# Optimization experiments

Measured on AMD Instinct MI355X. Metric: run time of the kernel, lower is better.

The kernel has to match this reference:

```python
import jax, jax.numpy as jnp
import numpy as np

N_RES = 4096
N_PAIRS = 500000

def setup_inputs() -> dict:
    key = jax.random.key(0)
    k1, k2, k3 = jax.random.split(key, 3)
    ca_coords = jax.random.normal(k1, (N_RES, 3), dtype=jnp.float32) * 10.0
    K = jax.random.uniform(k2, (N_RES, N_RES), dtype=jnp.float32)
    pairs = jax.random.randint(k3, (N_PAIRS, 2), 0, N_RES, dtype=jnp.int64)
    return {"ca_coords": ca_coords, "K": K, "pairs": pairs}


def _reconstruct_backbone(ca):
    # vectorized version of reconstruct_backbone_atoms
    n = ca.shape[0]
    vec = ca[1:] - ca[:-1]                                  # (n-1,3)
    unit = vec / (jnp.linalg.norm(vec, axis=-1, keepdims=True) + 1e-8)
    # N atoms: n_coords[i] = ca[i] - 0.38*unit(ca[i]-ca[i-1]); n_coords[0] uses unit[0]
    n_coords = jnp.concatenate([ca[:1] - 0.38 * unit[:1], ca[1:] - 0.38 * unit], axis=0)
    # C atoms: c_coords[i] = ca[i] + 0.38*unit(ca[i+1]-ca[i]); c_coords[-1] uses unit[-1]
    c_coords = jnp.concatenate([ca[:-1] + 0.38 * unit, ca[-1:] + 0.38 * unit[-1:]], axis=0)
    # O atoms: perpendicular to (C-CA, N-CA) plane, last residue special-cased
    vec_n = n_coords[:-1] - ca[:-1]
    vec_c = c_coords[:-1] - ca[:-1]
    perp = jnp.cross(vec_c, vec_n)
    pnorm = jnp.linalg.norm(perp, axis=-1, keepdims=True)
    perp = jnp.where(pnorm > 1e-6, perp / jnp.maximum(pnorm, 1e-12), perp)
    o_body = c_coords[:-1] + 1.24 * perp
    o_last = c_coords[-1:] + jnp.array([[0.0, 1.24, 0.0]], dtype=ca.dtype)
    o_coords = jnp.concatenate([o_body, o_last], axis=0)
    return n_coords, c_coords, o_coords


def _pairwise_dist(x, y):
    # safe cdist: sqrt clamped so diagonal zeros stay differentiable
    sq = jnp.sum((x[:, None, :] - y[None, :, :]) ** 2, axis=-1)
    return jnp.sqrt(jnp.maximum(sq, 1e-12))


def reference(ca_coords, K, pairs):
    n = ca_coords.shape[0]

    # --- bond energy (weight=30): mean((|ca[i+1]-ca[i]| - 3.8)^2) ---
    d_bond = jnp.linalg.norm(ca_coords[1:] - ca_coords[:-1], axis=-1)
    e_bond = 30.0 * jnp.mean((d_bond - 3.8) ** 2)

    # --- clash energy (weight=50): mean(relu(3.2 - d_pair)^2) ---
    dv = ca_coords[pairs[:, 0]] - ca_coords[pairs[:, 1]]
    d_pair = jnp.sqrt(jnp.maximum(jnp.sum(dv ** 2, axis=-1), 1e-12))
    e_clash = 50.0 * jnp.mean(jax.nn.relu(3.2 - d_pair) ** 2)

    # --- contact energy (weight=5): mean((D - 8*(1-K))^2) over full NxN ---
    D = _pairwise_dist(ca_coords, ca_coords)
    target = 8.0 * (1.0 - K)
    e_contact = 5.0 * jnp.mean((D - target) ** 2)

    # --- hydrogen bond energy (weight=4) from reconstructed backbone ---
    n_coords, c_coords, o_coords = _reconstruct_backbone(ca_coords)
    ideal = 2.95
    hb = jnp.float32(0.0)
    # double loop i, j in [i+2, i+6) -> offsets 2..5, vectorized per offset
    for off in (2, 3, 4, 5):
        d = jnp.linalg.norm(o_coords[: n - off] - n_coords[off:], axis=-1)
        pen = jnp.exp(-(((d - ideal) / 0.3) ** 2))
        hb = hb - 0.5 * jnp.sum(jnp.where((d > 2.5) & (d < 3.5), pen, 0.0))
    e_hb = 4.0 * hb / (n * n)

    return e_bond + e_clash + e_contact + e_hb
```

## Files before the change

kernel.cpp:

```cpp
#include <hip/hip_runtime.h>
#include <math.h>

#define NRES   4096
#define TROWS  8
#define GRID   (NRES / TROWS)
#define HB_BLOCKS (NRES / 256)
#define PSTRIDE (GRID * 256)

typedef int i32x2 __attribute__((ext_vector_type(2)));

__device__ __forceinline__ float wave_sum(float v) {
#pragma unroll
    for (int off = 32; off > 0; off >>= 1) v += __shfl_down(v, off, 64);
    return v;
}

__device__ __forceinline__ float fsqrt(float x) { return __builtin_amdgcn_sqrtf(x); }

__device__ __forceinline__ float c4(float4 kv, float4 cx, float4 cy, float4 cz,
                                    float xi, float yi, float zi, float s) {
    float dx, dy, dz, D, t;
    dx = xi - cx.x; dy = yi - cy.x; dz = zi - cz.x;
    D  = fsqrt(fmaf(dx, dx, fmaf(dy, dy, dz * dz)));
    t  = fmaf(8.f, kv.x, D - 8.f);
    s  = fmaf(t, t, s);

    dx = xi - cx.y; dy = yi - cy.y; dz = zi - cz.y;
    D  = fsqrt(fmaf(dx, dx, fmaf(dy, dy, dz * dz)));
    t  = fmaf(8.f, kv.y, D - 8.f);
    s  = fmaf(t, t, s);

    dx = xi - cx.z; dy = yi - cy.z; dz = zi - cz.z;
    D  = fsqrt(fmaf(dx, dx, fmaf(dy, dy, dz * dz)));
    t  = fmaf(8.f, kv.z, D - 8.f);
    s  = fmaf(t, t, s);

    dx = xi - cx.w; dy = yi - cy.w; dz = zi - cz.w;
    D  = fsqrt(fmaf(dx, dx, fmaf(dy, dy, dz * dz)));
    t  = fmaf(8.f, kv.w, D - 8.f);
    s  = fmaf(t, t, s);
    return s;
}

__global__ __launch_bounds__(256, 2) void energy_kernel(const float* __restrict__ ca,
                                                        const float* __restrict__ K,
                                                        const int* __restrict__ pairs,
                                                        float4* __restrict__ partial,
                                                        int npairs) {
    __shared__ float sx[NRES], sy[NRES], sz[NRES];
    __shared__ float red[4][4];
    const int tid = threadIdx.x;
    const int b   = blockIdx.x;

    const int rbase = b * TROWS;
    const float* Kt = K + (size_t)rbase * NRES;
    const int j0 = tid << 2;

    float4 va[TROWS], vb[TROWS];
#pragma unroll
    for (int r = 0; r < TROWS; ++r)
        va[r] = *(const float4*)(Kt + (size_t)r * NRES + j0);

    const int pbase = b * 256 + tid;
    const i32x2* pairs2 = (const i32x2*)pairs;
    i32x2 pr0 = pairs2[pbase];
    i32x2 pr1 = pairs2[pbase + PSTRIDE];
    i32x2 pr2 = pairs2[pbase + 2 * PSTRIDE];
    const bool has3 = (pbase + 3 * PSTRIDE) < npairs;
    i32x2 pr3 = has3 ? pairs2[pbase + 3 * PSTRIDE] : (i32x2){0, 0};

    for (int j = tid; j < NRES; j += 256) {
        sx[j] = ca[3 * j + 0];
        sy[j] = ca[3 * j + 1];
        sz[j] = ca[3 * j + 2];
    }
    __syncthreads();

    float xi[TROWS], yi[TROWS], zi[TROWS];
#pragma unroll
    for (int r = 0; r < TROWS; ++r) {
        xi[r] = sx[rbase + r]; yi[r] = sy[rbase + r]; zi[r] = sz[rbase + r];
    }

    float contact = 0.f, contact2 = 0.f;
#pragma unroll
    for (int c = 0; c < 4; ++c) {
        const int jc = j0 + (c << 10);
        float4* cur = (c & 1) ? vb : va;
        float4* nxt = (c & 1) ? va : vb;
        if (c < 3) {
            const int jn = j0 + ((c + 1) << 10);
#pragma unroll
            for (int r = 0; r < TROWS; ++r)
                nxt[r] = *(const float4*)(Kt + (size_t)r * NRES + jn);
        }
        const float4 cx = *(const float4*)&sx[jc];
        const float4 cy = *(const float4*)&sy[jc];
        const float4 cz = *(const float4*)&sz[jc];
#pragma unroll
        for (int r = 0; r < TROWS; r += 2) {
            contact  = c4(cur[r],     cx, cy, cz, xi[r],     yi[r],     zi[r],     contact);
            contact2 = c4(cur[r + 1], cx, cy, cz, xi[r + 1], yi[r + 1], zi[r + 1], contact2);
        }
    }
    contact += contact2;

    float clash = 0.f;
    {
        float dx, dy, dz, d, r;
        dx = sx[pr0.x] - sx[pr0.y]; dy = sy[pr0.x] - sy[pr0.y]; dz = sz[pr0.x] - sz[pr0.y];
        d = fsqrt(fmaxf(fmaf(dx, dx, fmaf(dy, dy, dz * dz)), 1e-12f));
        r = fmaxf(3.2f - d, 0.f); clash = fmaf(r, r, clash);

        dx = sx[pr1.x] - sx[pr1.y]; dy = sy[pr1.x] - sy[pr1.y]; dz = sz[pr1.x] - sz[pr1.y];
        d = fsqrt(fmaxf(fmaf(dx, dx, fmaf(dy, dy, dz * dz)), 1e-12f));
        r = fmaxf(3.2f - d, 0.f); clash = fmaf(r, r, clash);

        dx = sx[pr2.x] - sx[pr2.y]; dy = sy[pr2.x] - sy[pr2.y]; dz = sz[pr2.x] - sz[pr2.y];
        d = fsqrt(fmaxf(fmaf(dx, dx, fmaf(dy, dy, dz * dz)), 1e-12f));
        r = fmaxf(3.2f - d, 0.f); clash = fmaf(r, r, clash);

        if (has3) {
            dx = sx[pr3.x] - sx[pr3.y]; dy = sy[pr3.x] - sy[pr3.y]; dz = sz[pr3.x] - sz[pr3.y];
            d = fsqrt(fmaxf(fmaf(dx, dx, fmaf(dy, dy, dz * dz)), 1e-12f));
            r = fmaxf(3.2f - d, 0.f); clash = fmaf(r, r, clash);
        }
    }

    float bond = 0.f, hb = 0.f;
    if (b < HB_BLOCKS) {
        const int i = b * 256 + tid;
        const int n = NRES;

        if (i < n - 1) {
            float dx = sx[i+1]-sx[i], dy = sy[i+1]-sy[i], dz = sz[i+1]-sz[i];
            float d  = sqrtf(fmaf(dx, dx, fmaf(dy, dy, dz * dz)));
            float t  = d - 3.8f;
            bond = t * t;
        }

        if (i < n - 2) {
            float cax = sx[i], cay = sy[i], caz = sz[i];
            float vx = sx[i+1]-cax, vy = sy[i+1]-cay, vz = sz[i+1]-caz;
            float inv = 1.f / (sqrtf(vx*vx + vy*vy + vz*vz) + 1e-8f);
            float ux = vx*inv, uy = vy*inv, uz = vz*inv;

            float upx, upy, upz;
            if (i == 0) { upx = ux; upy = uy; upz = uz; }
            else {
                float wx = cax-sx[i-1], wy = cay-sy[i-1], wz = caz-sz[i-1];
                float inv2 = 1.f / (sqrtf(wx*wx + wy*wy + wz*wz) + 1e-8f);
                upx = wx*inv2; upy = wy*inv2; upz = wz*inv2;
            }

            float vcx = 0.38f*ux,  vcy = 0.38f*uy,  vcz = 0.38f*uz;
            float vnx = -0.38f*upx, vny = -0.38f*upy, vnz = -0.38f*upz;
            float px = vcy*vnz - vcz*vny;
            float py = vcz*vnx - vcx*vnz;
            float pz = vcx*vny - vcy*vnx;
            float pn = sqrtf(px*px + py*py + pz*pz);
            if (pn > 1e-6f) {
                float ipn = 1.f / fmaxf(pn, 1e-12f);
                px *= ipn; py *= ipn; pz *= ipn;
            }
            float ox = cax + vcx + 1.24f*px;
            float oy = cay + vcy + 1.24f*py;
            float oz = caz + vcz + 1.24f*pz;

#pragma unroll
            for (int off = 2; off <= 5; ++off) {
                int jj = i + off;
                if (jj < n) {
                    float cjx = sx[jj], cjy = sy[jj], cjz = sz[jj];
                    float qx = cjx-sx[jj-1], qy = cjy-sy[jj-1], qz = cjz-sz[jj-1];
                    float invq = 1.f / (sqrtf(qx*qx + qy*qy + qz*qz) + 1e-8f);
                    float njx = cjx - 0.38f*qx*invq;
                    float njy = cjy - 0.38f*qy*invq;
                    float njz = cjz - 0.38f*qz*invq;
                    float ddx = ox-njx, ddy = oy-njy, ddz = oz-njz;
                    float d = sqrtf(ddx*ddx + ddy*ddy + ddz*ddz);
                    if (d > 2.5f && d < 3.5f) {
                        float z = (d - 2.95f) * (1.0f / 0.3f);
                        hb -= 0.5f * expf(-z*z);
                    }
                }
            }
        }
    }

    float vbo = wave_sum(bond);
    float vcl = wave_sum(clash);
    float vco = wave_sum(contact);
    float vhb = wave_sum(hb);
    const int wave = tid >> 6;
    if ((tid & 63) == 0) {
        red[wave][0] = vbo; red[wave][1] = vcl; red[wave][2] = vco; red[wave][3] = vhb;
    }
    __syncthreads();
    if (tid == 0) {
        float4 o;
        o.x = red[0][0] + red[1][0] + red[2][0] + red[3][0];
        o.y = red[0][1] + red[1][1] + red[2][1] + red[3][1];
        o.z = red[0][2] + red[1][2] + red[2][2] + red[3][2];
        o.w = red[0][3] + red[1][3] + red[2][3] + red[3][3];
        partial[b] = o;
    }
}

__global__ __launch_bounds__(256) void finalize_kernel(const float4* __restrict__ partial,
                                                       float* __restrict__ out,
                                                       int n, int npairs) {
    __shared__ float red[4][4];
    const int tid = threadIdx.x;
    float vb = 0.f, vc = 0.f, vk = 0.f, vh = 0.f;
#pragma unroll
    for (int s = 0; s < GRID; s += 256) {
        float4 a = partial[tid + s];
        vb += a.x; vc += a.y; vk += a.z; vh += a.w;
    }
    vb = wave_sum(vb); vc = wave_sum(vc); vk = wave_sum(vk); vh = wave_sum(vh);
    const int wave = tid >> 6;
    if ((tid & 63) == 0) {
        red[wave][0] = vb; red[wave][1] = vc; red[wave][2] = vk; red[wave][3] = vh;
    }
    __syncthreads();
    if (tid == 0) {
        float bond    = red[0][0] + red[1][0] + red[2][0] + red[3][0];
        float clash   = red[0][1] + red[1][1] + red[2][1] + red[3][1];
        float contact = red[0][2] + red[1][2] + red[2][2] + red[3][2];
        float hb      = red[0][3] + red[1][3] + red[2][3] + red[3][3];
        float inv_nn  = 1.f / ((float)n * (float)n);
        out[0] = 30.f * bond / (float)(n - 1)
               + 50.f * clash / (float)npairs
               + 5.f  * contact * inv_nn
               + 4.f  * hb * inv_nn;
    }
}

extern "C" void kernel_launch(void* const* d_in, const int* in_sizes, int n_in,
                              void* d_out, int out_size, void* d_ws, size_t ws_size,
                              hipStream_t stream) {
    const float* ca    = (const float*)d_in[0];
    const float* K     = (const float*)d_in[1];
    const int*   pairs = (const int*)d_in[2];
    float* out = (float*)d_out;
    float4* partial = (float4*)d_ws;

    int n      = in_sizes[0] / 3;
    int npairs = in_sizes[2] / 2;

    energy_kernel<<<GRID, 256, 0, stream>>>(ca, K, pairs, partial, npairs);
    finalize_kernel<<<1, 256, 0, stream>>>(partial, out, n, npairs);
}
```

Measured before the change: 101.8 us.

## Drop shared-memory coordinate staging and halve rows per block

Removes the per-block copy of all 4096 CA coordinates into LDS and its barrier. Column coordinates are now read straight from global memory as float4 loads and de-interleaved in registers, while pair and H-bond lookups become global gathers. Rows per block drop from 8 to 4, which doubles the grid, and launch bounds are raised to allow more blocks per CU. The aim is to cut redundant LDS staging work and raise occupancy, at the cost of more global and cache traffic for the coordinate gathers.

```diff
diff --git a/kernel.cpp b/kernel.cpp
--- a/kernel.cpp
+++ b/kernel.cpp
@@ -2,7 +2,7 @@
 #include <math.h>
 
 #define NRES   4096
-#define TROWS  8
+#define TROWS  4
 #define GRID   (NRES / TROWS)
 #define HB_BLOCKS (NRES / 256)
 #define PSTRIDE (GRID * 256)
@@ -16,6 +16,11 @@
 }
 
 __device__ __forceinline__ float fsqrt(float x) { return __builtin_amdgcn_sqrtf(x); }
+
+__device__ __forceinline__ void ldp(const float* __restrict__ ca, int i,
+                                    float& x, float& y, float& z) {
+    x = ca[3 * i]; y = ca[3 * i + 1]; z = ca[3 * i + 2];
+}
 
 __device__ __forceinline__ float c4(float4 kv, float4 cx, float4 cy, float4 cz,
                                     float xi, float yi, float zi, float s) {
@@ -42,12 +47,11 @@
     return s;
 }
 
-__global__ __launch_bounds__(256, 2) void energy_kernel(const float* __restrict__ ca,
+__global__ __launch_bounds__(256, 4) void energy_kernel(const float* __restrict__ ca,
                                                         const float* __restrict__ K,
                                                         const int* __restrict__ pairs,
                                                         float4* __restrict__ partial,
                                                         int npairs) {
-    __shared__ float sx[NRES], sy[NRES], sz[NRES];
     __shared__ float red[4][4];
     const int tid = threadIdx.x;
     const int b   = blockIdx.x;
@@ -56,72 +60,67 @@
     const float* Kt = K + (size_t)rbase * NRES;
     const int j0 = tid << 2;
 
-    float4 va[TROWS], vb[TROWS];
+    float4 va[TROWS], vbuf[TROWS];
 #pragma unroll
     for (int r = 0; r < TROWS; ++r)
         va[r] = *(const float4*)(Kt + (size_t)r * NRES + j0);
+
+    float4 la[3], lb[3];
+#pragma unroll
+    for (int q = 0; q < 3; ++q)
+        la[q] = *(const float4*)(ca + 3 * j0 + 4 * q);
 
     const int pbase = b * 256 + tid;
     const i32x2* pairs2 = (const i32x2*)pairs;
     i32x2 pr0 = pairs2[pbase];
-    i32x2 pr1 = pairs2[pbase + PSTRIDE];
-    i32x2 pr2 = pairs2[pbase + 2 * PSTRIDE];
-    const bool has3 = (pbase + 3 * PSTRIDE) < npairs;
-    i32x2 pr3 = has3 ? pairs2[pbase + 3 * PSTRIDE] : (i32x2){0, 0};
-
-    for (int j = tid; j < NRES; j += 256) {
-        sx[j] = ca[3 * j + 0];
-        sy[j] = ca[3 * j + 1];
-        sz[j] = ca[3 * j + 2];
-    }
-    __syncthreads();
+    const bool has1 = (pbase + PSTRIDE) < npairs;
+    i32x2 pr1 = has1 ? pairs2[pbase + PSTRIDE] : (i32x2){0, 0};
 
     float xi[TROWS], yi[TROWS], zi[TROWS];
 #pragma unroll
-    for (int r = 0; r < TROWS; ++r) {
-        xi[r] = sx[rbase + r]; yi[r] = sy[rbase + r]; zi[r] = sz[rbase + r];
-    }
+    for (int r = 0; r < TROWS; ++r)
+        ldp(ca, rbase + r, xi[r], yi[r], zi[r]);
 
     float contact = 0.f, contact2 = 0.f;
 #pragma unroll
     for (int c = 0; c < 4; ++c) {
-        const int jc = j0 + (c << 10);
-        float4* cur = (c & 1) ? vb : va;
-        float4* nxt = (c & 1) ? va : vb;
+        float4* cur  = (c & 1) ? vbuf : va;
+        float4* nxt  = (c & 1) ? va : vbuf;
+        float4* curc = (c & 1) ? lb : la;
+        float4* nxtc = (c & 1) ? la : lb;
         if (c < 3) {
             const int jn = j0 + ((c + 1) << 10);
 #pragma unroll
             for (int r = 0; r < TROWS; ++r)
                 nxt[r] = *(const float4*)(Kt + (size_t)r * NRES + jn);
-        }
-        const float4 cx = *(const float4*)&sx[jc];
-        const float4 cy = *(const float4*)&sy[jc];
-        const float4 cz = *(const float4*)&sz[jc];
-#pragma unroll
-        for (int r = 0; r < TROWS; r += 2) {
-            contact  = c4(cur[r],     cx, cy, cz, xi[r],     yi[r],     zi[r],     contact);
-            contact2 = c4(cur[r + 1], cx, cy, cz, xi[r + 1], yi[r + 1], zi[r + 1], contact2);
-        }
+#pragma unroll
+            for (int q = 0; q < 3; ++q)
+                nxtc[q] = *(const float4*)(ca + 3 * jn + 4 * q);
+        }
+        const float4 cx = make_float4(curc[0].x, curc[0].w, curc[1].z, curc[2].y);
+        const float4 cy = make_float4(curc[0].y, curc[1].x, curc[1].w, curc[2].z);
+        const float4 cz = make_float4(curc[0].z, curc[1].y, curc[2].x, curc[2].w);
+
+        contact  = c4(cur[0], cx, cy, cz, xi[0], yi[0], zi[0], contact);
+        contact2 = c4(cur[1], cx, cy, cz, xi[1], yi[1], zi[1], contact2);
+        contact  = c4(cur[2], cx, cy, cz, xi[2], yi[2], zi[2], contact);
+        contact2 = c4(cur[3], cx, cy, cz, xi[3], yi[3], zi[3], contact2);
     }
     contact += contact2;
 
     float clash = 0.f;
     {
-        float dx, dy, dz, d, r;
-        dx = sx[pr0.x] - sx[pr0.y]; dy = sy[pr0.x] - sy[pr0.y]; dz = sz[pr0.x] - sz[pr0.y];
+        float ax, ay, az, bx, by, bz, dx, dy, dz, d, r;
+        ldp(ca, pr0.x, ax, ay, az);
+        ldp(ca, pr0.y, bx, by, bz);
+        dx = ax - bx; dy = ay - by; dz = az - bz;
         d = fsqrt(fmaxf(fmaf(dx, dx, fmaf(dy, dy, dz * dz)), 1e-12f));
         r = fmaxf(3.2f - d, 0.f); clash = fmaf(r, r, clash);
 
-        dx = sx[pr1.x] - sx[pr1.y]; dy = sy[pr1.x] - sy[pr1.y]; dz = sz[pr1.x] - sz[pr1.y];
-        d = fsqrt(fmaxf(fmaf(dx, dx, fmaf(dy, dy, dz * dz)), 1e-12f));
-        r = fmaxf(3.2f - d, 0.f); clash = fmaf(r, r, clash);
-
-        dx = sx[pr2.x] - sx[pr2.y]; dy = sy[pr2.x] - sy[pr2.y]; dz = sz[pr2.x] - sz[pr2.y];
-        d = fsqrt(fmaxf(fmaf(dx, dx, fmaf(dy, dy, dz * dz)), 1e-12f));
-        r = fmaxf(3.2f - d, 0.f); clash = fmaf(r, r, clash);
-
-        if (has3) {
-            dx = sx[pr3.x] - sx[pr3.y]; dy = sy[pr3.x] - sy[pr3.y]; dz = sz[pr3.x] - sz[pr3.y];
+        if (has1) {
+            ldp(ca, pr1.x, ax, ay, az);
+            ldp(ca, pr1.y, bx, by, bz);
+            dx = ax - bx; dy = ay - by; dz = az - bz;
             d = fsqrt(fmaxf(fmaf(dx, dx, fmaf(dy, dy, dz * dz)), 1e-12f));
             r = fmaxf(3.2f - d, 0.f); clash = fmaf(r, r, clash);
         }
@@ -132,23 +131,28 @@
         const int i = b * 256 + tid;
         const int n = NRES;
 
+        float cax, cay, caz, nx1, ny1, nz1;
+        ldp(ca, i, cax, cay, caz);
+
         if (i < n - 1) {
-            float dx = sx[i+1]-sx[i], dy = sy[i+1]-sy[i], dz = sz[i+1]-sz[i];
+            ldp(ca, i + 1, nx1, ny1, nz1);
+            float dx = nx1 - cax, dy = ny1 - cay, dz = nz1 - caz;
             float d  = sqrtf(fmaf(dx, dx, fmaf(dy, dy, dz * dz)));
             float t  = d - 3.8f;
             bond = t * t;
         }
 
         if (i < n - 2) {
-            float cax = sx[i], cay = sy[i], caz = sz[i];
-            float vx = sx[i+1]-cax, vy = sy[i+1]-cay, vz = sz[i+1]-caz;
+            float vx = nx1 - cax, vy = ny1 - cay, vz = nz1 - caz;
             float inv = 1.f / (sqrtf(vx*vx + vy*vy + vz*vz) + 1e-8f);
             float ux = vx*inv, uy = vy*inv, uz = vz*inv;
 
             float upx, upy, upz;
             if (i == 0) { upx = ux; upy = uy; upz = uz; }
             else {
-                float wx = cax-sx[i-1], wy = cay-sy[i-1], wz = caz-sz[i-1];
+                float mx, my, mz;
+                ldp(ca, i - 1, mx, my, mz);
+                float wx = cax-mx, wy = cay-my, wz = caz-mz;
                 float inv2 = 1.f / (sqrtf(wx*wx + wy*wy + wz*wz) + 1e-8f);
                 upx = wx*inv2; upy = wy*inv2; upz = wz*inv2;
             }
@@ -167,12 +171,15 @@
             float oy = cay + vcy + 1.24f*py;
             float oz = caz + vcz + 1.24f*pz;
 
+            float pjx, pjy, pjz;
+            pjx = nx1; pjy = ny1; pjz = nz1;
 #pragma unroll
             for (int off = 2; off <= 5; ++off) {
                 int jj = i + off;
                 if (jj < n) {
-                    float cjx = sx[jj], cjy = sy[jj], cjz = sz[jj];
-                    float qx = cjx-sx[jj-1], qy = cjy-sy[jj-1], qz = cjz-sz[jj-1];
+                    float cjx, cjy, cjz;
+                    ldp(ca, jj, cjx, cjy, cjz);
+                    float qx = cjx-pjx, qy = cjy-pjy, qz = cjz-pjz;
                     float invq = 1.f / (sqrtf(qx*qx + qy*qy + qz*qz) + 1e-8f);
                     float njx = cjx - 0.38f*qx*invq;
                     float njy = cjy - 0.38f*qy*invq;
@@ -183,6 +190,7 @@
                         float z = (d - 2.95f) * (1.0f / 0.3f);
                         hb -= 0.5f * expf(-z*z);
                     }
+                    pjx = cjx; pjy = cjy; pjz = cjz;
                 }
             }
         }
```

Result: slower. 114.0 us (+12.0%).

## Fuse finalize into main kernel via last-block ticket and deepen K prefetch

Applied to the files above, without the earlier changes.

Replaces the separate finalize launch with a global atomic ticket. The last block to finish reads all partials through volatile loads, reduces them, writes the output and resets the counter. This removes a second kernel launch and its dependency gap. The K-tile prefetch also changes to keep two chunks in flight and load each next chunk after computing on the current one. The ticket adds an atomic and fences per block and relies on the counter being reset correctly between calls.

```diff
diff --git a/kernel.cpp b/kernel.cpp
--- a/kernel.cpp
+++ b/kernel.cpp
@@ -9,6 +9,8 @@
 
 typedef int i32x2 __attribute__((ext_vector_type(2)));
 
+__device__ int g_ticket = 0;
+
 __device__ __forceinline__ float wave_sum(float v) {
 #pragma unroll
     for (int off = 32; off > 0; off >>= 1) v += __shfl_down(v, off, 64);
@@ -46,9 +48,11 @@
                                                         const float* __restrict__ K,
                                                         const int* __restrict__ pairs,
                                                         float4* __restrict__ partial,
+                                                        float* __restrict__ out,
                                                         int npairs) {
     __shared__ float sx[NRES], sy[NRES], sz[NRES];
     __shared__ float red[4][4];
+    __shared__ int lastflag;
     const int tid = threadIdx.x;
     const int b   = blockIdx.x;
 
@@ -56,10 +60,13 @@
     const float* Kt = K + (size_t)rbase * NRES;
     const int j0 = tid << 2;
 
-    float4 va[TROWS], vb[TROWS];
+    float4 va[TROWS], vbuf[TROWS];
 #pragma unroll
     for (int r = 0; r < TROWS; ++r)
         va[r] = *(const float4*)(Kt + (size_t)r * NRES + j0);
+#pragma unroll
+    for (int r = 0; r < TROWS; ++r)
+        vbuf[r] = *(const float4*)(Kt + (size_t)r * NRES + j0 + 1024);
 
     const int pbase = b * 256 + tid;
     const i32x2* pairs2 = (const i32x2*)pairs;
@@ -85,15 +92,8 @@
     float contact = 0.f, contact2 = 0.f;
 #pragma unroll
     for (int c = 0; c < 4; ++c) {
+        float4* cur = (c & 1) ? vbuf : va;
         const int jc = j0 + (c << 10);
-        float4* cur = (c & 1) ? vb : va;
-        float4* nxt = (c & 1) ? va : vb;
-        if (c < 3) {
-            const int jn = j0 + ((c + 1) << 10);
-#pragma unroll
-            for (int r = 0; r < TROWS; ++r)
-                nxt[r] = *(const float4*)(Kt + (size_t)r * NRES + jn);
-        }
         const float4 cx = *(const float4*)&sx[jc];
         const float4 cy = *(const float4*)&sy[jc];
         const float4 cz = *(const float4*)&sz[jc];
@@ -101,6 +101,12 @@
         for (int r = 0; r < TROWS; r += 2) {
             contact  = c4(cur[r],     cx, cy, cz, xi[r],     yi[r],     zi[r],     contact);
             contact2 = c4(cur[r + 1], cx, cy, cz, xi[r + 1], yi[r + 1], zi[r + 1], contact2);
+        }
+        if (c < 2) {
+            const int jn = j0 + ((c + 2) << 10);
+#pragma unroll
+            for (int r = 0; r < TROWS; ++r)
+                cur[r] = *(const float4*)(Kt + (size_t)r * NRES + jn);
         }
     }
     contact += contact2;
@@ -204,36 +210,40 @@
         o.z = red[0][2] + red[1][2] + red[2][2] + red[3][2];
         o.w = red[0][3] + red[1][3] + red[2][3] + red[3][3];
         partial[b] = o;
-    }
-}
-
-__global__ __launch_bounds__(256) void finalize_kernel(const float4* __restrict__ partial,
-                                                       float* __restrict__ out,
-                                                       int n, int npairs) {
-    __shared__ float red[4][4];
-    const int tid = threadIdx.x;
-    float vb = 0.f, vc = 0.f, vk = 0.f, vh = 0.f;
-#pragma unroll
-    for (int s = 0; s < GRID; s += 256) {
-        float4 a = partial[tid + s];
-        vb += a.x; vc += a.y; vk += a.z; vh += a.w;
-    }
-    vb = wave_sum(vb); vc = wave_sum(vc); vk = wave_sum(vk); vh = wave_sum(vh);
-    const int wave = tid >> 6;
-    if ((tid & 63) == 0) {
-        red[wave][0] = vb; red[wave][1] = vc; red[wave][2] = vk; red[wave][3] = vh;
+        __threadfence();
+        int old = atomicAdd(&g_ticket, 1);
+        lastflag = (old == GRID - 1);
     }
     __syncthreads();
-    if (tid == 0) {
-        float bond    = red[0][0] + red[1][0] + red[2][0] + red[3][0];
-        float clash   = red[0][1] + red[1][1] + red[2][1] + red[3][1];
-        float contact = red[0][2] + red[1][2] + red[2][2] + red[3][2];
-        float hb      = red[0][3] + red[1][3] + red[2][3] + red[3][3];
-        float inv_nn  = 1.f / ((float)n * (float)n);
-        out[0] = 30.f * bond / (float)(n - 1)
-               + 50.f * clash / (float)npairs
-               + 5.f  * contact * inv_nn
-               + 4.f  * hb * inv_nn;
+
+    if (lastflag) {
+        __threadfence();
+        const volatile float* pv = (const volatile float*)partial;
+        float fb = 0.f, fc = 0.f, fk = 0.f, fh = 0.f;
+#pragma unroll
+        for (int s = 0; s < GRID; s += 256) {
+            const int idx = (tid + s) << 2;
+            fb += pv[idx + 0]; fc += pv[idx + 1]; fk += pv[idx + 2]; fh += pv[idx + 3];
+        }
+        fb = wave_sum(fb); fc = wave_sum(fc); fk = wave_sum(fk); fh = wave_sum(fh);
+        __syncthreads();
+        if ((tid & 63) == 0) {
+            red[wave][0] = fb; red[wave][1] = fc; red[wave][2] = fk; red[wave][3] = fh;
+        }
+        __syncthreads();
+        if (tid == 0) {
+            float bondS    = red[0][0] + red[1][0] + red[2][0] + red[3][0];
+            float clashS   = red[0][1] + red[1][1] + red[2][1] + red[3][1];
+            float contactS = red[0][2] + red[1][2] + red[2][2] + red[3][2];
+            float hbS      = red[0][3] + red[1][3] + red[2][3] + red[3][3];
+            const float n  = (float)NRES;
+            float inv_nn   = 1.f / (n * n);
+            out[0] = 30.f * bondS / (n - 1.f)
+                   + 50.f * clashS / (float)npairs
+                   + 5.f  * contactS * inv_nn
+                   + 4.f  * hbS * inv_nn;
+            g_ticket = 0;
+        }
     }
 }
 
@@ -246,9 +256,7 @@
     float* out = (float*)d_out;
     float4* partial = (float4*)d_ws;
 
-    int n      = in_sizes[0] / 3;
     int npairs = in_sizes[2] / 2;
 
-    energy_kernel<<<GRID, 256, 0, stream>>>(ca, K, pairs, partial, npairs);
-    finalize_kernel<<<1, 256, 0, stream>>>(partial, out, n, npairs);
-}
+    energy_kernel<<<GRID, 256, 0, stream>>>(ca, K, pairs, partial, out, npairs);
+}
```

Result: slower. 113.1 us (+11.1%).
